# Performance work log

Hardware: AMD Instinct MI355X
Metric: run time of the kernel (lower is better)

## Reference

```python
import jax, jax.numpy as jnp
import numpy as np
from jax.ops import segment_sum

N_NODES = 100000
N_EDGES = 1600000
N_LABEL = 200000
IN_C, HID_C, OUT_C = 128, 128, 64


def setup_inputs() -> dict:
    key = jax.random.key(0)
    ks = jax.random.split(key, 6)
    x = jax.random.normal(ks[0], (N_NODES, IN_C), dtype=jnp.float32)
    edge_index = jax.random.randint(ks[1], (2, N_EDGES), 0, N_NODES, dtype=jnp.int64)
    edge_label_index = jax.random.randint(ks[2], (2, N_LABEL), 0, N_NODES, dtype=jnp.int64)
    W1 = jax.random.normal(ks[3], (IN_C, HID_C), dtype=jnp.float32) / np.sqrt(IN_C)
    b1 = jnp.zeros((HID_C,), dtype=jnp.float32)
    W2 = jax.random.normal(ks[4], (HID_C, OUT_C), dtype=jnp.float32) / np.sqrt(HID_C)
    b2 = jnp.zeros((OUT_C,), dtype=jnp.float32)
    return {"x": x, "edge_index": edge_index, "edge_label_index": edge_label_index,
            "W1": W1, "b1": b1, "W2": W2, "b2": b2}


def gcn_conv(x, W, b, src, dst, num_nodes):
    # PyG GCNConv: linear transform, add self-loops, symmetric normalization, sum-aggregate, bias.
    h = x @ W                                            # [N, C_out]
    loop = jnp.arange(num_nodes, dtype=src.dtype)
    s = jnp.concatenate([src, loop])                     # [E + N]
    d = jnp.concatenate([dst, loop])
    deg = segment_sum(jnp.ones_like(d, dtype=h.dtype), d, num_segments=num_nodes)
    dinv = jnp.where(deg > 0, jax.lax.rsqrt(deg), 0.0)   # deg^-1/2
    norm = dinv[s] * dinv[d]                             # [E + N]
    msg = h[s] * norm[:, None]                           # gather + scale
    out = segment_sum(msg, d, num_segments=num_nodes)    # scatter-add aggregate
    return out + b


def reference(x, edge_index, edge_label_index, W1, b1, W2, b2):
    src, dst = edge_index[0], edge_index[1]
    n = x.shape[0]
    h = jax.nn.relu(gcn_conv(x, W1, b1, src, dst, n))
    z = gcn_conv(h, W2, b2, src, dst, n)                 # encode
    # decode: dot product over candidate edges
    return jnp.sum(z[edge_label_index[0]] * z[edge_label_index[1]], axis=-1)
```

## Files before the change

### kernel.cpp

```cpp
#include <hip/hip_runtime.h>

typedef __attribute__((ext_vector_type(8))) short bfrag8;
typedef __attribute__((ext_vector_type(4))) float facc4;

__device__ __forceinline__ unsigned int f2bf(float f) {
    unsigned int u = __float_as_uint(f);
    return (u + 0x7FFFu + ((u >> 16) & 1u)) >> 16;
}
__device__ __forceinline__ float bf_lo(unsigned int w) { return __uint_as_float(w << 16); }
__device__ __forceinline__ float bf_hi(unsigned int w) { return __uint_as_float(w & 0xffff0000u); }


#define CNT_G 192

__global__ void k_prep(const float* __restrict__ x, const float* __restrict__ W1,
                       const float* __restrict__ W2, unsigned short* __restrict__ x16,
                       unsigned short* __restrict__ w1t, unsigned short* __restrict__ w2t,
                       const int* __restrict__ dst, int* __restrict__ cnt,
                       int e, int nx8, float scale) {
    int b = blockIdx.x;
    if (b < 8 * CNT_G) {
        int r = b & 7, g = b >> 3;
        int chunk = (e + CNT_G - 1) / CNT_G;
        int beg = g * chunk, end = min(beg + chunk, e);
        for (int i = beg + threadIdx.x; i < end; i += blockDim.x) {
            int d = dst[i];
            if ((int)((float)d * scale) == r) atomicAdd(&cnt[d], 1);
        }
        return;
    }
    int t = (b - 8 * CNT_G) * blockDim.x + threadIdx.x;
    if (t < nx8) {
        const float4* xp = reinterpret_cast<const float4*>(x) + (long)t * 2;
        float4 a = xp[0], v = xp[1];
        uint4 o;
        o.x = f2bf(a.x) | (f2bf(a.y) << 16);
        o.y = f2bf(a.z) | (f2bf(a.w) << 16);
        o.z = f2bf(v.x) | (f2bf(v.y) << 16);
        o.w = f2bf(v.z) | (f2bf(v.w) << 16);
        reinterpret_cast<uint4*>(x16)[t] = o;
    } else {
        int u = t - nx8;
        if (u < 128 * 128) {
            int k = u >> 7, nn = u & 127;
            w1t[nn * 128 + k] = (unsigned short)f2bf(W1[u]);
        } else if ((u -= 128 * 128) < 128 * 64) {
            int k = u >> 6, nn = u & 63;
            w2t[nn * 128 + k] = (unsigned short)f2bf(W2[u]);
        }
    }
}

#define SCP 1024

__global__ void k_scan_a(const int* __restrict__ cnt, int* __restrict__ part, int n) {
    int p = blockIdx.x * blockDim.x + threadIdx.x;
    if (p >= SCP) return;
    int chunk = (n + SCP - 1) / SCP;
    int b = p * chunk, e = min(b + chunk, n), s = 0;
    for (int i = b; i < e; ++i) s += cnt[i];
    part[p] = s;
}

__global__ void k_scan_b(int* __restrict__ part) {
    __shared__ int sm[SCP];
    int t = threadIdx.x;
    sm[t] = part[t];
    __syncthreads();
    for (int off = 1; off < SCP; off <<= 1) {
        int v = (t >= off) ? sm[t - off] : 0;
        __syncthreads();
        sm[t] += v;
        __syncthreads();
    }
    part[t] = t ? sm[t - 1] : 0;
}

__global__ void k_scan_c(const int* __restrict__ cnt, const int* __restrict__ part,
                         int* __restrict__ rowptr, int* __restrict__ cursor,
                         float* __restrict__ dinv, int n) {
    int p = blockIdx.x * blockDim.x + threadIdx.x;
    if (p >= SCP) return;
    int chunk = (n + SCP - 1) / SCP;
    int b = p * chunk, e = min(b + chunk, n);
    int run = part[p];
    for (int i = b; i < e; ++i) {
        rowptr[i] = run;
        cursor[i] = run;
        dinv[i] = rsqrtf((float)(cnt[i] + 1));
        run += cnt[i];
    }
    if (p == SCP - 1) rowptr[n] = run;
}


#define FILL_G 192

__device__ __forceinline__ void fill_role(const int* __restrict__ src,
                                          const int* __restrict__ dstv,
                                          int* __restrict__ cursor,
                                          int* __restrict__ csr_src,
                                          int e, float scale, int r, int g) {
    int chunk = (e + FILL_G - 1) / FILL_G;
    int beg = g * chunk, end = min(beg + chunk, e);
    for (int i = beg + threadIdx.x; i < end; i += blockDim.x) {
        int d = dstv[i];
        if ((int)((float)d * scale) == r) {
            int pos = atomicAdd(&cursor[d], 1);
            csr_src[pos] = src[i];
        }
    }
}


__global__ __launch_bounds__(256) void k_fuse(
        const int* __restrict__ src, const int* __restrict__ dstv,
        int* __restrict__ cursor, int* __restrict__ csr_src, int e, float scale,
        const unsigned short* __restrict__ X16, const unsigned short* __restrict__ W1T,
        const float* __restrict__ dinv, unsigned short* __restrict__ H16, int n) {
    __shared__ unsigned short sA[128 * 64];
    __shared__ unsigned short sB[128 * 64];

    int t8 = blockIdx.x >> 3, l8 = blockIdx.x & 7;
    int m = t8 % 3, q = t8 / 3;

    if (m < 2) {
        int g = q * 2 + m;
        if (g < FILL_G)
            fill_role(src, dstv, cursor, csr_src, e, scale, l8, g);
        return;
    }

    int bid = q * 8 + l8;
    int row0 = bid * 128;
    if (row0 >= n) return;

    int tid = threadIdx.x;
    int lane = tid & 63;
    int wv = tid >> 6;

    facc4 acc[2][8];
#pragma unroll
    for (int i = 0; i < 2; ++i)
#pragma unroll
        for (int j = 0; j < 8; ++j) acc[i][j] = (facc4)0.f;

    for (int s = 0; s < 2; ++s) {
        if (s) __syncthreads();
#pragma unroll
        for (int it = 0; it < 4; ++it) {
            int chunk = it * 4 + wv;
            int L = chunk * 64 + lane;
            int row = L >> 3, gp = L & 7;
            int gsrc = gp ^ (row & 7);
            int grow = min(row0 + row, n - 1);
            const unsigned short* srcp = X16 + (long)grow * 128 + s * 64 + gsrc * 8;
            unsigned short* dstp = sA + chunk * 512;
            __builtin_amdgcn_global_load_lds(
                (const __attribute__((address_space(1))) void*)srcp,
                (__attribute__((address_space(3))) void*)dstp, 16, 0, 0);
        }
#pragma unroll
        for (int it = 0; it < 4; ++it) {
            int chunk = it * 4 + wv;
            int L = chunk * 64 + lane;
            int row = L >> 3, gp = L & 7;
            int gsrc = gp ^ (row & 7);
            const unsigned short* srcp = W1T + (long)row * 128 + s * 64 + gsrc * 8;
            unsigned short* dstp = sB + chunk * 512;
            __builtin_amdgcn_global_load_lds(
                (const __attribute__((address_space(1))) void*)srcp,
                (__attribute__((address_space(3))) void*)dstp, 16, 0, 0);
        }
        __syncthreads();

        bfrag8 af[2][2];
#pragma unroll
        for (int mt = 0; mt < 2; ++mt)
#pragma unroll
            for (int ks = 0; ks < 2; ++ks) {
                int r = wv * 32 + mt * 16 + (lane & 15);
                int g = ks * 4 + (lane >> 4);
                af[mt][ks] = *reinterpret_cast<const bfrag8*>(&sA[r * 64 + (g ^ (r & 7)) * 8]);
            }
#pragma unroll
        for (int nt = 0; nt < 8; ++nt) {
            int nr = nt * 16 + (lane & 15);
            bfrag8 b0 = *reinterpret_cast<const bfrag8*>(&sB[nr * 64 + (((lane >> 4)) ^ (nr & 7)) * 8]);
            bfrag8 b1 = *reinterpret_cast<const bfrag8*>(&sB[nr * 64 + ((4 + (lane >> 4)) ^ (nr & 7)) * 8]);
            acc[0][nt] = __builtin_amdgcn_mfma_f32_16x16x32_bf16(af[0][0], b0, acc[0][nt], 0, 0, 0);
            acc[1][nt] = __builtin_amdgcn_mfma_f32_16x16x32_bf16(af[1][0], b0, acc[1][nt], 0, 0, 0);
            acc[0][nt] = __builtin_amdgcn_mfma_f32_16x16x32_bf16(af[0][1], b1, acc[0][nt], 0, 0, 0);
            acc[1][nt] = __builtin_amdgcn_mfma_f32_16x16x32_bf16(af[1][1], b1, acc[1][nt], 0, 0, 0);
        }
    }

#pragma unroll
    for (int mt = 0; mt < 2; ++mt)
#pragma unroll
        for (int reg = 0; reg < 4; ++reg) {
            int r = row0 + wv * 32 + mt * 16 + (lane >> 4) * 4 + reg;
            if (r < n) {
                float dv = dinv[r];
#pragma unroll
                for (int nt = 0; nt < 8; ++nt)
                    H16[(long)r * 128 + nt * 16 + (lane & 15)] =
                        (unsigned short)f2bf(acc[mt][nt][reg] * dv);
            }
        }
}


__global__ __launch_bounds__(256) void k_gemmM64(const unsigned short* __restrict__ H16,
                                                 const unsigned short* __restrict__ W2T,
                                                 const float* __restrict__ dinv,
                                                 unsigned short* __restrict__ Z16, int n) {
    __shared__ unsigned short sA[128 * 64];
    __shared__ unsigned short sB[64 * 64];

    int row0 = blockIdx.x * 128;
    int tid = threadIdx.x;
    int lane = tid & 63;
    int wv = tid >> 6;

    facc4 acc[2][4];
#pragma unroll
    for (int i = 0; i < 2; ++i)
#pragma unroll
        for (int j = 0; j < 4; ++j) acc[i][j] = (facc4)0.f;

    for (int s = 0; s < 2; ++s) {
        if (s) __syncthreads();
#pragma unroll
        for (int it = 0; it < 4; ++it) {
            int chunk = it * 4 + wv;
            int L = chunk * 64 + lane;
            int row = L >> 3, gp = L & 7;
            int gsrc = gp ^ (row & 7);
            int grow = min(row0 + row, n - 1);
            const unsigned short* srcp = H16 + (long)grow * 128 + s * 64 + gsrc * 8;
            unsigned short* dstp = sA + chunk * 512;
            __builtin_amdgcn_global_load_lds(
                (const __attribute__((address_space(1))) void*)srcp,
                (__attribute__((address_space(3))) void*)dstp, 16, 0, 0);
        }
#pragma unroll
        for (int it = 0; it < 2; ++it) {
            int chunk = it * 4 + wv;
            int L = chunk * 64 + lane;
            int row = L >> 3, gp = L & 7;
            int gsrc = gp ^ (row & 7);
            const unsigned short* srcp = W2T + (long)row * 128 + s * 64 + gsrc * 8;
            unsigned short* dstp = sB + chunk * 512;
            __builtin_amdgcn_global_load_lds(
                (const __attribute__((address_space(1))) void*)srcp,
                (__attribute__((address_space(3))) void*)dstp, 16, 0, 0);
        }
        __syncthreads();

        bfrag8 af[2][2];
#pragma unroll
        for (int mt = 0; mt < 2; ++mt)
#pragma unroll
            for (int ks = 0; ks < 2; ++ks) {
                int r = wv * 32 + mt * 16 + (lane & 15);
                int g = ks * 4 + (lane >> 4);
                af[mt][ks] = *reinterpret_cast<const bfrag8*>(&sA[r * 64 + (g ^ (r & 7)) * 8]);
            }
#pragma unroll
        for (int nt = 0; nt < 4; ++nt) {
            int nr = nt * 16 + (lane & 15);
            bfrag8 b0 = *reinterpret_cast<const bfrag8*>(&sB[nr * 64 + (((lane >> 4)) ^ (nr & 7)) * 8]);
            bfrag8 b1 = *reinterpret_cast<const bfrag8*>(&sB[nr * 64 + ((4 + (lane >> 4)) ^ (nr & 7)) * 8]);
            acc[0][nt] = __builtin_amdgcn_mfma_f32_16x16x32_bf16(af[0][0], b0, acc[0][nt], 0, 0, 0);
            acc[1][nt] = __builtin_amdgcn_mfma_f32_16x16x32_bf16(af[1][0], b0, acc[1][nt], 0, 0, 0);
            acc[0][nt] = __builtin_amdgcn_mfma_f32_16x16x32_bf16(af[0][1], b1, acc[0][nt], 0, 0, 0);
            acc[1][nt] = __builtin_amdgcn_mfma_f32_16x16x32_bf16(af[1][1], b1, acc[1][nt], 0, 0, 0);
        }
    }

#pragma unroll
    for (int mt = 0; mt < 2; ++mt)
#pragma unroll
        for (int reg = 0; reg < 4; ++reg) {
            int r = row0 + wv * 32 + mt * 16 + (lane >> 4) * 4 + reg;
            if (r < n) {
                float dv = dinv[r];
#pragma unroll
                for (int nt = 0; nt < 4; ++nt)
                    Z16[(long)r * 64 + nt * 16 + (lane & 15)] =
                        (unsigned short)f2bf(acc[mt][nt][reg] * dv);
            }
        }
}


template<int C, bool RELU, bool OB>
__global__ void k_gather16(const int* __restrict__ rowptr, const int* __restrict__ csr_src,
                           const float* __restrict__ dinv, const unsigned short* __restrict__ h16,
                           const float* __restrict__ bias, void* __restrict__ outv, int n) {
    const int TPN = C / 8;
    const int RS = C / 8;
    int t = blockIdx.x * blockDim.x + threadIdx.x;
    int node = t / TPN;
    if (node >= n) return;
    int cg = t % TPN;

    const uint4* h4 = reinterpret_cast<const uint4*>(h16);
    float acc[8];
    {
        uint4 u = h4[(long)node * RS + cg];
        acc[0] = bf_lo(u.x); acc[1] = bf_hi(u.x);
        acc[2] = bf_lo(u.y); acc[3] = bf_hi(u.y);
        acc[4] = bf_lo(u.z); acc[5] = bf_hi(u.z);
        acc[6] = bf_lo(u.w); acc[7] = bf_hi(u.w);
    }

    int beg = rowptr[node], end = rowptr[node + 1];
    int e = beg;
    for (; e + 8 <= end; e += 8) {
        int s[8];
#pragma unroll
        for (int q = 0; q < 8; ++q) s[q] = csr_src[e + q];
        uint4 u[8];
#pragma unroll
        for (int q = 0; q < 8; ++q) u[q] = h4[(long)s[q] * RS + cg];
#pragma unroll
        for (int q = 0; q < 8; ++q) {
            acc[0] += bf_lo(u[q].x); acc[1] += bf_hi(u[q].x);
            acc[2] += bf_lo(u[q].y); acc[3] += bf_hi(u[q].y);
            acc[4] += bf_lo(u[q].z); acc[5] += bf_hi(u[q].z);
            acc[6] += bf_lo(u[q].w); acc[7] += bf_hi(u[q].w);
        }
    }
    for (; e < end; ++e) {
        uint4 u = h4[(long)csr_src[e] * RS + cg];
        acc[0] += bf_lo(u.x); acc[1] += bf_hi(u.x);
        acc[2] += bf_lo(u.y); acc[3] += bf_hi(u.y);
        acc[4] += bf_lo(u.z); acc[5] += bf_hi(u.z);
        acc[6] += bf_lo(u.w); acc[7] += bf_hi(u.w);
    }

    float dd = dinv[node];
    int c0 = cg * 8;
    float4 ba = *reinterpret_cast<const float4*>(bias + c0);
    float4 bb = *reinterpret_cast<const float4*>(bias + c0 + 4);
    float o[8];
    o[0] = fmaf(acc[0], dd, ba.x); o[1] = fmaf(acc[1], dd, ba.y);
    o[2] = fmaf(acc[2], dd, ba.z); o[3] = fmaf(acc[3], dd, ba.w);
    o[4] = fmaf(acc[4], dd, bb.x); o[5] = fmaf(acc[5], dd, bb.y);
    o[6] = fmaf(acc[6], dd, bb.z); o[7] = fmaf(acc[7], dd, bb.w);
    if (RELU) {
#pragma unroll
        for (int i = 0; i < 8; ++i) o[i] = fmaxf(o[i], 0.f);
    }
    if (OB) {
        uint4 w;
        w.x = f2bf(o[0]) | (f2bf(o[1]) << 16);
        w.y = f2bf(o[2]) | (f2bf(o[3]) << 16);
        w.z = f2bf(o[4]) | (f2bf(o[5]) << 16);
        w.w = f2bf(o[6]) | (f2bf(o[7]) << 16);
        *reinterpret_cast<uint4*>((unsigned short*)outv + (long)node * C + c0) = w;
    } else {
        float* of = (float*)outv + (long)node * C + c0;
        *reinterpret_cast<float4*>(of) = make_float4(o[0], o[1], o[2], o[3]);
        *reinterpret_cast<float4*>(of + 4) = make_float4(o[4], o[5], o[6], o[7]);
    }
}


__global__ void k_decode16(const int* __restrict__ ia, const int* __restrict__ ib,
                           const unsigned short* __restrict__ z, float* __restrict__ out, int m) {
    int t = blockIdx.x * blockDim.x + threadIdx.x;
    int k = t >> 3;
    if (k >= m) return;
    int cg = t & 7;
    int a = ia[k], b = ib[k];
    const uint4* z4 = reinterpret_cast<const uint4*>(z);
    uint4 ua = z4[(long)a * 8 + cg];
    uint4 ub = z4[(long)b * 8 + cg];
    float dot = bf_lo(ua.x) * bf_lo(ub.x) + bf_hi(ua.x) * bf_hi(ub.x)
              + bf_lo(ua.y) * bf_lo(ub.y) + bf_hi(ua.y) * bf_hi(ub.y)
              + bf_lo(ua.z) * bf_lo(ub.z) + bf_hi(ua.z) * bf_hi(ub.z)
              + bf_lo(ua.w) * bf_lo(ub.w) + bf_hi(ua.w) * bf_hi(ub.w);
    dot += __shfl_xor(dot, 4);
    dot += __shfl_xor(dot, 2);
    dot += __shfl_xor(dot, 1);
    if (cg == 0) out[k] = dot;
}


extern "C" void kernel_launch(void* const* d_in, const int* in_sizes, int n_in,
                              void* d_out, int out_size, void* d_ws, size_t ws_size,
                              hipStream_t stream) {
    const float* x  = (const float*)d_in[0];
    const int*   ei = (const int*)d_in[1];
    const int*   el = (const int*)d_in[2];
    const float* W1 = (const float*)d_in[3];
    const float* b1 = (const float*)d_in[4];
    const float* W2 = (const float*)d_in[5];
    const float* b2 = (const float*)d_in[6];
    float* out = (float*)d_out;

    const int N = in_sizes[0] / 128;
    const int E = in_sizes[1] / 2;
    const int L = out_size;

    const int* src = ei;
    const int* dst = ei + E;
    const int* la  = el;
    const int* lb  = el + L;

    char* wsb = (char*)d_ws;

    unsigned short* ht16 = (unsigned short*)wsb;
    unsigned short* zt16 = (unsigned short*)wsb;
    unsigned short* z16  = (unsigned short*)(wsb + (size_t)N * 256);

    unsigned short* h16  = (unsigned short*)(wsb + (size_t)N * 512);
    unsigned short* x16  = (unsigned short*)(wsb + (size_t)N * 512 + (size_t)N * 256);

    int*   csr_src = (int*)(wsb + (size_t)N * 1024);
    int*   cnt     = csr_src + E;
    int*   rowptr  = cnt + N;
    int*   cursor  = rowptr + N + 1;
    float* dinv    = (float*)(cursor + N);
    int*   part    = (int*)(dinv + N);
    unsigned short* w1t = (unsigned short*)(part + SCP);
    unsigned short* w2t = w1t + 128 * 128;

    auto cdiv = [](long a, long b) { return (int)((a + b - 1) / b); };

    hipMemsetAsync(cnt, 0, (size_t)N * sizeof(int), stream);
    int nx8 = N * 16;
    int cvtB = cdiv((long)nx8 + 128 * 128 + 128 * 64, 256);
    k_prep<<<8 * CNT_G + cvtB, 256, 0, stream>>>(x, W1, W2, x16, w1t, w2t,
                                                 dst, cnt, E, nx8, 8.0f / (float)N);

    k_scan_a<<<SCP / 256, 256, 0, stream>>>(cnt, part, N);
    k_scan_b<<<1, SCP, 0, stream>>>(part);
    k_scan_c<<<SCP / 256, 256, 0, stream>>>(cnt, part, rowptr, cursor, dinv, N);

    k_fuse<<<294 * 8, 256, 0, stream>>>(src, dst, cursor, csr_src, E, 8.0f / (float)N,
                                        x16, w1t, dinv, ht16, N);

    k_gather16<128, true, true><<<cdiv((long)N * 16, 256), 256, 0, stream>>>(
        rowptr, csr_src, dinv, ht16, b1, h16, N);

    k_gemmM64<<<cdiv(N, 128), 256, 0, stream>>>(h16, w2t, dinv, zt16, N);
    k_gather16<64, false, true><<<cdiv((long)N * 8, 256), 256, 0, stream>>>(
        rowptr, csr_src, dinv, zt16, b2, z16, N);

    k_decode16<<<cdiv((long)L * 8, 256), 256, 0, stream>>>(la, lb, z16, out, L);
}
```

Baseline: 352.2 us.

## Record per-edge rank during degree count to replace fill-phase atomics

```diff
diff --git a/kernel.cpp b/kernel.cpp
--- a/kernel.cpp
+++ b/kernel.cpp
@@ -11,25 +11,23 @@
 __device__ __forceinline__ float bf_hi(unsigned int w) { return __uint_as_float(w & 0xffff0000u); }
 
 
-#define CNT_G 192
+#define CNT_B 2048
 
 __global__ void k_prep(const float* __restrict__ x, const float* __restrict__ W1,
                        const float* __restrict__ W2, unsigned short* __restrict__ x16,
                        unsigned short* __restrict__ w1t, unsigned short* __restrict__ w2t,
                        const int* __restrict__ dst, int* __restrict__ cnt,
-                       int e, int nx8, float scale) {
+                       unsigned int* __restrict__ pack, int e, int nx8) {
     int b = blockIdx.x;
-    if (b < 8 * CNT_G) {
-        int r = b & 7, g = b >> 3;
-        int chunk = (e + CNT_G - 1) / CNT_G;
-        int beg = g * chunk, end = min(beg + chunk, e);
-        for (int i = beg + threadIdx.x; i < end; i += blockDim.x) {
+    if (b < CNT_B) {
+        for (int i = b * 256 + threadIdx.x; i < e; i += CNT_B * 256) {
             int d = dst[i];
-            if ((int)((float)d * scale) == r) atomicAdd(&cnt[d], 1);
+            int r = atomicAdd(&cnt[d], 1);
+            pack[i] = ((unsigned int)d << 14) | (unsigned int)r;
         }
         return;
     }
-    int t = (b - 8 * CNT_G) * blockDim.x + threadIdx.x;
+    int t = (b - CNT_B) * 256 + threadIdx.x;
     if (t < nx8) {
         const float4* xp = reinterpret_cast<const float4*>(x) + (long)t * 2;
         float4 a = xp[0], v = xp[1];
@@ -77,8 +75,7 @@
 }
 
 __global__ void k_scan_c(const int* __restrict__ cnt, const int* __restrict__ part,
-                         int* __restrict__ rowptr, int* __restrict__ cursor,
-                         float* __restrict__ dinv, int n) {
+                         int* __restrict__ rowptr, float* __restrict__ dinv, int n) {
     int p = blockIdx.x * blockDim.x + threadIdx.x;
     if (p >= SCP) return;
     int chunk = (n + SCP - 1) / SCP;
@@ -86,7 +83,6 @@
     int run = part[p];
     for (int i = b; i < e; ++i) {
         rowptr[i] = run;
-        cursor[i] = run;
         dinv[i] = rsqrtf((float)(cnt[i] + 1));
         run += cnt[i];
     }
@@ -97,16 +93,17 @@
 #define FILL_G 192
 
 __device__ __forceinline__ void fill_role(const int* __restrict__ src,
-                                          const int* __restrict__ dstv,
-                                          int* __restrict__ cursor,
+                                          const unsigned int* __restrict__ pack,
+                                          const int* __restrict__ rowptr,
                                           int* __restrict__ csr_src,
                                           int e, float scale, int r, int g) {
     int chunk = (e + FILL_G - 1) / FILL_G;
     int beg = g * chunk, end = min(beg + chunk, e);
     for (int i = beg + threadIdx.x; i < end; i += blockDim.x) {
-        int d = dstv[i];
+        unsigned int p = pack[i];
+        int d = (int)(p >> 14);
         if ((int)((float)d * scale) == r) {
-            int pos = atomicAdd(&cursor[d], 1);
+            int pos = rowptr[d] + (int)(p & 0x3FFFu);
             csr_src[pos] = src[i];
         }
     }
@@ -114,8 +111,8 @@
 
 
 __global__ __launch_bounds__(256) void k_fuse(
-        const int* __restrict__ src, const int* __restrict__ dstv,
-        int* __restrict__ cursor, int* __restrict__ csr_src, int e, float scale,
+        const int* __restrict__ src, const unsigned int* __restrict__ pack,
+        const int* __restrict__ rowptr, int* __restrict__ csr_src, int e, float scale,
         const unsigned short* __restrict__ X16, const unsigned short* __restrict__ W1T,
         const float* __restrict__ dinv, unsigned short* __restrict__ H16, int n) {
     __shared__ unsigned short sA[128 * 64];
@@ -127,7 +124,7 @@
     if (m < 2) {
         int g = q * 2 + m;
         if (g < FILL_G)
-            fill_role(src, dstv, cursor, csr_src, e, scale, l8, g);
+            fill_role(src, pack, rowptr, csr_src, e, scale, l8, g);
         return;
     }
 
@@ -417,14 +414,14 @@
     unsigned short* zt16 = (unsigned short*)wsb;
     unsigned short* z16  = (unsigned short*)(wsb + (size_t)N * 256);
 
+    unsigned int*   pack = (unsigned int*)(wsb + (size_t)N * 512);
     unsigned short* h16  = (unsigned short*)(wsb + (size_t)N * 512);
     unsigned short* x16  = (unsigned short*)(wsb + (size_t)N * 512 + (size_t)N * 256);
 
     int*   csr_src = (int*)(wsb + (size_t)N * 1024);
     int*   cnt     = csr_src + E;
     int*   rowptr  = cnt + N;
-    int*   cursor  = rowptr + N + 1;
-    float* dinv    = (float*)(cursor + N);
+    float* dinv    = (float*)(rowptr + N + 1);
     int*   part    = (int*)(dinv + N);
     unsigned short* w1t = (unsigned short*)(part + SCP);
     unsigned short* w2t = w1t + 128 * 128;
@@ -434,14 +431,14 @@
     hipMemsetAsync(cnt, 0, (size_t)N * sizeof(int), stream);
     int nx8 = N * 16;
     int cvtB = cdiv((long)nx8 + 128 * 128 + 128 * 64, 256);
-    k_prep<<<8 * CNT_G + cvtB, 256, 0, stream>>>(x, W1, W2, x16, w1t, w2t,
-                                                 dst, cnt, E, nx8, 8.0f / (float)N);
+    k_prep<<<CNT_B + cvtB, 256, 0, stream>>>(x, W1, W2, x16, w1t, w2t,
+                                             dst, cnt, pack, E, nx8);
 
     k_scan_a<<<SCP / 256, 256, 0, stream>>>(cnt, part, N);
     k_scan_b<<<1, SCP, 0, stream>>>(part);
-    k_scan_c<<<SCP / 256, 256, 0, stream>>>(cnt, part, rowptr, cursor, dinv, N);
-
-    k_fuse<<<294 * 8, 256, 0, stream>>>(src, dst, cursor, csr_src, E, 8.0f / (float)N,
+    k_scan_c<<<SCP / 256, 256, 0, stream>>>(cnt, part, rowptr, dinv, N);
+
+    k_fuse<<<294 * 8, 256, 0, stream>>>(src, pack, rowptr, csr_src, E, 8.0f / (float)N,
                                         x16, w1t, dinv, ht16, N);
 
     k_gather16<128, true, true><<<cdiv((long)N * 16, 256), 256, 0, stream>>>(
```

Measured after the change: 318.9 us. 9.5% less time.
